# Kernel tuning notes

Hardware: AMD Instinct MI355X
Metric: run time of the kernel (lower is better)

## Reference

```python
import jax, jax.numpy as jnp
import numpy as np

T, B, D, H = 1024, 8, 1024, 16
NH = D // H  # 64, per-head width (nhid)
W_SCALE = 0.02


def setup_inputs() -> dict:
    key = jax.random.key(0)
    ks = jax.random.split(key, 10)
    return {
        "input_tensor": jax.random.normal(ks[0], (T, B, D), jnp.float32),
        "keys_vector": jax.random.normal(ks[1], (T, B, D), jnp.float32),
        "values_vector": jax.random.normal(ks[2], (T, B, D), jnp.float32),
        # per-head projection weights: [H, D, NH]
        "Wq": jax.random.normal(ks[3], (H, D, NH), jnp.float32) * W_SCALE,
        "bq": jnp.zeros((H, NH), jnp.float32),
        "Wk": jax.random.normal(ks[4], (H, D, NH), jnp.float32) * W_SCALE,
        "bk": jnp.zeros((H, NH), jnp.float32),
        "Wv": jax.random.normal(ks[5], (H, D, NH), jnp.float32) * W_SCALE,
        "bv": jnp.zeros((H, NH), jnp.float32),
        # output projection after concatenating heads
        "Wo": jax.random.normal(ks[6], (D, D), jnp.float32) * W_SCALE,
        "bo": jnp.zeros((D,), jnp.float32),
        "mask": 1,  # True: causal (growing key slice per timestep)
    }


def reference(input_tensor, keys_vector, values_vector, Wq, bq, Wk, bk, Wv, bv, Wo, bo, mask):
    # Vectorized equivalent of the per-timestep loop: query at step t attends
    # to keys/values[:t+1] when mask is set, else to the full sequence.
    q = jnp.einsum('tbd,hdk->tbhk', input_tensor, Wq) + bq   # [T,B,H,NH]
    k = jnp.einsum('sbd,hdk->sbhk', keys_vector, Wk) + bk    # [T,B,H,NH]
    v = jnp.einsum('sbd,hdk->sbhk', values_vector, Wv) + bv  # [T,B,H,NH]

    scale = 1.0 / jnp.sqrt(jnp.float32(NH))
    scores = jnp.einsum('tbhk,sbhk->bhts', q, k) * scale     # [B,H,T,T]
    if mask:
        causal = jnp.tril(jnp.ones((T, T), dtype=bool))      # s <= t
        scores = jnp.where(causal[None, None], scores, jnp.float32(-1e9))
    attn = jax.nn.softmax(scores, axis=-1)                   # over key dim s

    out = jnp.einsum('bhts,sbhk->tbhk', attn, v)             # [T,B,H,NH]
    out = out.reshape(T, B, D)                               # concat heads
    return out @ Wo.T + bo                                   # [T,B,D]
```

## Files before the change

### kernel.cpp

```cpp
#include <hip/hip_runtime.h>

typedef short bf16x8 __attribute__((ext_vector_type(8)));
typedef float f32x4 __attribute__((ext_vector_type(4)));
typedef float f32x16 __attribute__((ext_vector_type(16)));

typedef const __attribute__((address_space(1))) void* gptr_t;
typedef __attribute__((address_space(3))) void* sptr_t;

#define Z16 {0.f,0.f,0.f,0.f,0.f,0.f,0.f,0.f,0.f,0.f,0.f,0.f,0.f,0.f,0.f,0.f}
#define VMCNT(n) asm volatile("s_waitcnt vmcnt(" #n ")" ::: "memory")
#define LGKM0 asm volatile("s_waitcnt lgkmcnt(0)" ::: "memory")
#define SCHEDB __builtin_amdgcn_sched_barrier(0)
#define SBAR __builtin_amdgcn_s_barrier()

__device__ __forceinline__ void glds16(const void* g, void* s) {
  __builtin_amdgcn_global_load_lds((gptr_t)g, (sptr_t)s, 16, 0, 0);
}

__device__ __forceinline__ unsigned short f2bf(float x) {
  unsigned u = __float_as_uint(x);
  u = u + 0x7fffu + ((u >> 16) & 1u);
  return (unsigned short)(u >> 16);
}

__device__ __forceinline__ unsigned packbf(float lo, float hi) {
  return (unsigned)f2bf(lo) | (((unsigned)f2bf(hi)) << 16);
}

__global__ void cvtall(const float* __restrict__ X, const float* __restrict__ KY,
                       const float* __restrict__ VY, const float* __restrict__ Wo,
                       unsigned short* __restrict__ XB, unsigned short* __restrict__ WOB) {
  int stride = gridDim.x * blockDim.x;
  for (int i = blockIdx.x * blockDim.x + threadIdx.x; i < 6553600; i += stride) {
    const float* in; unsigned short* out; int k;
    if (i < 2097152)      { in = X;  out = XB;            k = i; }
    else if (i < 4194304) { in = KY; out = XB + 8388608;  k = i - 2097152; }
    else if (i < 6291456) { in = VY; out = XB + 16777216; k = i - 4194304; }
    else                  { in = Wo; out = WOB;           k = i - 6291456; }
    float4 v = ((const float4*)in)[k];
    uint2 r;
    r.x = packbf(v.x, v.y);
    r.y = packbf(v.z, v.w);
    ((uint2*)out)[k] = r;
  }
}

__global__ __launch_bounds__(256) void wtrans(const float* __restrict__ Wq,
                                              const float* __restrict__ Wk,
                                              const float* __restrict__ Wv,
                                              unsigned short* __restrict__ WT) {
  int m = blockIdx.y >> 4, h = blockIdx.y & 15, d0 = blockIdx.x * 64;
  const float* src = (m == 0 ? Wq : (m == 1 ? Wk : Wv)) + (size_t)h * 65536;
  __shared__ float tile[64][65];
  int c = (threadIdx.x & 15) * 4, r0 = threadIdx.x >> 4;
#pragma unroll
  for (int rr = 0; rr < 4; ++rr) {
    int dr = rr * 16 + r0;
    float4 v = *(const float4*)(src + (size_t)(d0 + dr) * 64 + c);
    tile[dr][c + 0] = v.x; tile[dr][c + 1] = v.y;
    tile[dr][c + 2] = v.z; tile[dr][c + 3] = v.w;
  }
  __syncthreads();
#pragma unroll
  for (int rr = 0; rr < 4; ++rr) {
    int kr = rr * 16 + r0;
    uint2 pk;
    pk.x = packbf(tile[c + 0][kr], tile[c + 1][kr]);
    pk.y = packbf(tile[c + 2][kr], tile[c + 3][kr]);
    *(uint2*)(WT + ((size_t)(m * 1024 + h * 64 + kr)) * 1024 + d0 + c) = pk;
  }
}

__global__ __launch_bounds__(256) void gemm_qkv(const unsigned short* __restrict__ Ab,
                                                const unsigned short* __restrict__ Bb,
                                                const float* __restrict__ bi0,
                                                const float* __restrict__ bi1,
                                                const float* __restrict__ bi2,
                                                unsigned short* __restrict__ outp) {
  const int K = 1024;
  int z = blockIdx.z;
  const unsigned short* A = Ab + (size_t)z * 8192 * 1024;
  const unsigned short* BT = Bb + (size_t)z * 1024 * 1024;
  const float* bias = z == 0 ? bi0 : (z == 1 ? bi1 : bi2);
  int lin = blockIdx.y * 64 + blockIdx.x;
  int mt = (lin & 7) * 8 + ((lin >> 3) & 7);
  int nt = lin >> 6;
  int m0 = mt * 128, n0 = nt * 128;
  __shared__ __align__(16) char lds[65536];
  int tid = threadIdx.x, w = tid >> 6, l = tid & 63, ml = l & 15, hi = l >> 4;
  int wr = (w >> 1) * 64, wc = (w & 1) * 64;
  int srow = l >> 3;
  int kphys = (l & 7) << 4;
  f32x4 acc[4][4] = {};
#pragma unroll
  for (int i = 0; i < 4; ++i) {
    int c = w * 4 + i;
    int row = c * 8 + srow;
    int klog = kphys ^ ((row & 7) << 4);
    glds16((const char*)(A + (size_t)(m0 + row) * K) + klog, lds + c * 1024);
    glds16((const char*)(BT + (size_t)(n0 + row) * K) + klog, lds + 16384 + c * 1024);
  }
  __syncthreads();
  int cur = 0;
  for (int kt16 = 0; kt16 < 16; ++kt16) {
    if (kt16 + 1 < 16) {
      char* nb = lds + (cur ^ 1) * 32768;
      int kt = (kt16 + 1) * 64;
#pragma unroll
      for (int i = 0; i < 4; ++i) {
        int c = w * 4 + i;
        int row = c * 8 + srow;
        int klog = kphys ^ ((row & 7) << 4);
        glds16((const char*)(A + (size_t)(m0 + row) * K + kt) + klog, nb + c * 1024);
        glds16((const char*)(BT + (size_t)(n0 + row) * K + kt) + klog, nb + 16384 + c * 1024);
      }
    }
    char* As = lds + cur * 32768;
    char* Bs = As + 16384;
#pragma unroll
    for (int ks = 0; ks < 2; ++ks) {
      bf16x8 af[4], bfr[4];
#pragma unroll
      for (int mi = 0; mi < 4; ++mi) {
        int row = wr + mi * 16 + ml;
        af[mi] = *(const bf16x8*)(As + row * 128 + ((ks * 64 + (hi << 4)) ^ ((row & 7) << 4)));
      }
#pragma unroll
      for (int ni = 0; ni < 4; ++ni) {
        int row = wc + ni * 16 + ml;
        bfr[ni] = *(const bf16x8*)(Bs + row * 128 + ((ks * 64 + (hi << 4)) ^ ((row & 7) << 4)));
      }
      __builtin_amdgcn_s_setprio(1);
#pragma unroll
      for (int mi = 0; mi < 4; ++mi)
#pragma unroll
        for (int ni = 0; ni < 4; ++ni)
          acc[mi][ni] = __builtin_amdgcn_mfma_f32_16x16x32_bf16(af[mi], bfr[ni], acc[mi][ni], 0, 0, 0);
      __builtin_amdgcn_s_setprio(0);
    }
    __syncthreads();
    cur ^= 1;
  }
#pragma unroll
  for (int mi = 0; mi < 4; ++mi) {
#pragma unroll
    for (int ni = 0; ni < 4; ++ni) {
      int col = wc + ni * 16 + ml;
      float bv = bias[n0 + col];
#pragma unroll
      for (int r = 0; r < 4; ++r) {
        int row = wr + mi * 16 + (hi << 2) + r;
        float v = acc[mi][ni][r] + bv;
        float pv = __shfl_xor(v, 1);
        unsigned pk = (ml & 1) ? packbf(pv, v) : packbf(v, pv);
        *(unsigned*)(lds + row * 256 + (((col * 2) & ~3) ^ ((row & 7) << 4))) = pk;
      }
    }
  }
  __syncthreads();
  unsigned short* ob = outp + (size_t)z * 8388608;
  if (z != 2) {
    int rr = tid >> 1, hh = tid & 1;
    int t = (m0 + rr) >> 3, b = (m0 + rr) & 7;
    int hg = (n0 >> 6) + hh;
    unsigned short* dst = ob + (size_t)(b * 16 + hg) * 65536 + (size_t)t * 64;
#pragma unroll
    for (int j = 0; j < 8; ++j) {
      uint4 d = *(uint4*)(lds + rr * 256 + ((hh * 128 + j * 16) ^ ((rr & 7) << 4)));
      *(uint4*)(dst + j * 8) = d;
    }
  } else {
    int t0 = m0 >> 3;
#pragma unroll
    for (int q = 0; q < 4; ++q) {
      int run = q * 256 + tid;
      int k = run & 63;
      int bh2 = run >> 6;
      int b = bh2 >> 1, hh = bh2 & 1;
      int colb = (hh * 64 + k) * 2;
      union { unsigned short u[16]; uint4 v[2]; } tmp;
#pragma unroll
      for (int tp = 0; tp < 16; ++tp) {
        int rowt = tp * 8 + b;
        tmp.u[tp] = *(unsigned short*)(lds + rowt * 256 + (colb ^ ((b & 7) << 4)));
      }
      int hg = (n0 >> 6) + hh;
      unsigned short* dst = ob + (size_t)(b * 16 + hg) * 65536 + (size_t)k * 1024 + t0;
      *(uint4*)dst = tmp.v[0];
      *(uint4*)(dst + 8) = tmp.v[1];
    }
  }
}

__global__ __launch_bounds__(256) void gemm_out(const unsigned short* __restrict__ A,
                                                const unsigned short* __restrict__ BT,
                                                const float* __restrict__ bias,
                                                float* __restrict__ outp) {
  const int K = 1024;
  int lin = blockIdx.y * 64 + blockIdx.x;
  int mt = (lin & 7) * 8 + ((lin >> 3) & 7);
  int nt = lin >> 6;
  int m0 = mt * 128, n0 = nt * 128;
  __shared__ __align__(16) char lds[65536];
  int tid = threadIdx.x, w = tid >> 6, l = tid & 63, ml = l & 15, hi = l >> 4;
  int wr = (w >> 1) * 64, wc = (w & 1) * 64;
  int srow = l >> 3;
  int kphys = (l & 7) << 4;
  f32x4 acc[4][4] = {};
#pragma unroll
  for (int i = 0; i < 4; ++i) {
    int c = w * 4 + i;
    int row = c * 8 + srow;
    int klog = kphys ^ ((row & 7) << 4);
    glds16((const char*)(A + (size_t)(m0 + row) * K) + klog, lds + c * 1024);
    glds16((const char*)(BT + (size_t)(n0 + row) * K) + klog, lds + 16384 + c * 1024);
  }
  __syncthreads();
  int cur = 0;
  for (int kt16 = 0; kt16 < 16; ++kt16) {
    if (kt16 + 1 < 16) {
      char* nb = lds + (cur ^ 1) * 32768;
      int kt = (kt16 + 1) * 64;
#pragma unroll
      for (int i = 0; i < 4; ++i) {
        int c = w * 4 + i;
        int row = c * 8 + srow;
        int klog = kphys ^ ((row & 7) << 4);
        glds16((const char*)(A + (size_t)(m0 + row) * K + kt) + klog, nb + c * 1024);
        glds16((const char*)(BT + (size_t)(n0 + row) * K + kt) + klog, nb + 16384 + c * 1024);
      }
    }
    char* As = lds + cur * 32768;
    char* Bs = As + 16384;
#pragma unroll
    for (int ks = 0; ks < 2; ++ks) {
      bf16x8 af[4], bfr[4];
#pragma unroll
      for (int mi = 0; mi < 4; ++mi) {
        int row = wr + mi * 16 + ml;
        af[mi] = *(const bf16x8*)(As + row * 128 + ((ks * 64 + (hi << 4)) ^ ((row & 7) << 4)));
      }
#pragma unroll
      for (int ni = 0; ni < 4; ++ni) {
        int row = wc + ni * 16 + ml;
        bfr[ni] = *(const bf16x8*)(Bs + row * 128 + ((ks * 64 + (hi << 4)) ^ ((row & 7) << 4)));
      }
      __builtin_amdgcn_s_setprio(1);
#pragma unroll
      for (int mi = 0; mi < 4; ++mi)
#pragma unroll
        for (int ni = 0; ni < 4; ++ni)
          acc[mi][ni] = __builtin_amdgcn_mfma_f32_16x16x32_bf16(af[mi], bfr[ni], acc[mi][ni], 0, 0, 0);
      __builtin_amdgcn_s_setprio(0);
    }
    __syncthreads();
    cur ^= 1;
  }
#pragma unroll
  for (int mi = 0; mi < 4; ++mi) {
#pragma unroll
    for (int ni = 0; ni < 4; ++ni) {
      int col = n0 + wc + ni * 16 + ml;
      float bv = bias[col];
#pragma unroll
      for (int r = 0; r < 4; ++r) {
        int row = m0 + wr + mi * 16 + (hi << 2) + r;
        outp[(size_t)row * 1024 + col] = acc[mi][ni][r] + bv;
      }
    }
  }
}

__global__ __launch_bounds__(512, 4) void attn_k(const unsigned short* __restrict__ Qp,
                                                 const unsigned short* __restrict__ Kp,
                                                 const unsigned short* __restrict__ VTp,
                                                 unsigned short* __restrict__ Op,
                                                 const int* __restrict__ maskp) {
  int lin = blockIdx.x;
  int xcd = lin & 7, idx = lin >> 3;
  int bh = xcd + 8 * (idx >> 2);
  int j = idx & 3;
  const size_t base = (size_t)bh * 65536;
  int tid = threadIdx.x, w = tid >> 6, l = tid & 63;
  int ml5 = l & 31, hi1 = l >> 5;
  int half = w & 1, pi = w >> 1;
  int stripe = (pi == 0) ? j : (pi == 1) ? (15 - j) : (pi == 2) ? (7 - j) : (8 + j);
  int tw0 = stripe * 64 + half * 32;
  int t_glob = tw0 + ml5;
  __shared__ __align__(16) char lds[32768];
  int msk = *maskp;
  const float CE = 0.18033688011112042f;
  bf16x8 bq[4];
#pragma unroll
  for (int kd = 0; kd < 4; ++kd)
    bq[kd] = *(const bf16x8*)(Qp + base + (size_t)t_glob * 64 + kd * 16 + hi1 * 8);
  f32x16 o0 = Z16, o1 = Z16;
  float m_run = -3e38f, l_run = 0.f;
  int nt = msk ? (16 - j) : 16;
  int diag = stripe;
  int srow = l >> 3, kphys = (l & 7) << 4;
  int row = w * 8 + srow;
  int klog = kphys ^ (srow << 4);
  int swz = (ml5 & 7) << 4;
  glds16((const char*)(Kp + base + (size_t)row * 64) + klog, lds + w * 1024);
  glds16((const char*)(VTp + base + (size_t)row * 1024) + klog, lds + 8192 + w * 1024);
  int cur = 0;
  for (int st = 0; st < nt; ++st) {
    if (st + 1 < nt) {
      char* nb = lds + (cur ^ 1) * 16384;
      glds16((const char*)(Kp + base + (size_t)((st + 1) * 64 + row) * 64) + klog, nb + w * 1024);
      glds16((const char*)(VTp + base + (size_t)row * 1024 + (st + 1) * 64) + klog, nb + 8192 + w * 1024);
      VMCNT(4);
    } else {
      VMCNT(0);
    }
    SCHEDB; SBAR; SCHEDB;
    if (!msk || st <= diag) {
      char* Ks = lds + cur * 16384;
      char* Vs = Ks + 8192;
      f32x16 s0 = Z16, s1 = Z16;
      __builtin_amdgcn_s_setprio(1);
#pragma unroll
      for (int kd = 0; kd < 4; ++kd) {
        int koff = kd * 32 + hi1 * 16;
        bf16x8 a0 = *(const bf16x8*)(Ks + ml5 * 128 + (koff ^ swz));
        bf16x8 a1 = *(const bf16x8*)(Ks + (32 + ml5) * 128 + (koff ^ swz));
        s0 = __builtin_amdgcn_mfma_f32_32x32x16_bf16(a0, bq[kd], s0, 0, 0, 0);
        s1 = __builtin_amdgcn_mfma_f32_32x32x16_bf16(a1, bq[kd], s1, 0, 0, 0);
      }
      __builtin_amdgcn_s_setprio(0);
      if (msk && st == diag) {
#pragma unroll
        for (int r = 0; r < 16; ++r) {
          int sl = st * 64 + (r & 3) + 8 * (r >> 2) + 4 * hi1;
          if (sl > t_glob) s0[r] = -1e30f;
          if (sl + 32 > t_glob) s1[r] = -1e30f;
        }
      }
      float t8[8];
#pragma unroll
      for (int r = 0; r < 8; ++r)
        t8[r] = fmaxf(fmaxf(s0[r], s0[r + 8]), fmaxf(s1[r], s1[r + 8]));
      float tm = fmaxf(fmaxf(fmaxf(t8[0], t8[1]), fmaxf(t8[2], t8[3])),
                       fmaxf(fmaxf(t8[4], t8[5]), fmaxf(t8[6], t8[7])));
      tm = fmaxf(tm, __shfl_xor(tm, 32));
      if (!__all(tm <= m_run + 8.0f)) {
        float m_new = fmaxf(m_run, tm);
        float sc2 = exp2f((m_run - m_new) * CE);
        l_run *= sc2;
#pragma unroll
        for (int r = 0; r < 16; ++r) { o0[r] *= sc2; o1[r] *= sc2; }
        m_run = m_new;
      }
      float mC = m_run * CE;
#pragma unroll
      for (int r = 0; r < 16; ++r) {
        s0[r] = exp2f(fmaf(s0[r], CE, -mC));
        s1[r] = exp2f(fmaf(s1[r], CE, -mC));
      }
      float a8[8];
#pragma unroll
      for (int r = 0; r < 8; ++r)
        a8[r] = (s0[r] + s0[r + 8]) + (s1[r] + s1[r + 8]);
      float ps = ((a8[0] + a8[1]) + (a8[2] + a8[3])) + ((a8[4] + a8[5]) + (a8[6] + a8[7]));
      ps += __shfl_xor(ps, 32);
      l_run += ps;
      unsigned cc0[4][2], cc1[4][2];
#pragma unroll
      for (int q = 0; q < 4; ++q) {
        cc0[q][0] = packbf(s0[4 * q + 0], s0[4 * q + 1]);
        cc0[q][1] = packbf(s0[4 * q + 2], s0[4 * q + 3]);
        cc1[q][0] = packbf(s1[4 * q + 0], s1[4 * q + 1]);
        cc1[q][1] = packbf(s1[4 * q + 2], s1[4 * q + 3]);
      }
#define CCa(a, p) ((a) < 4 ? cc0[(a) & 3][p] : cc1[(a) & 3][p])
      union U4 { unsigned u[4]; bf16x8 v; };
      bf16x8 pb[4];
#pragma unroll
      for (int kb = 0; kb < 4; ++kb) {
        U4 t;
#pragma unroll
        for (int p = 0; p < 2; ++p) {
          unsigned x = CCa(2 * kb, p), y = CCa(2 * kb + 1, p);
          unsigned v = hi1 ? x : y;
          unsigned wv = hi1 ? y : x;
          unsigned vs = __shfl_xor(v, 32);
          t.u[p]     = hi1 ? vs : wv;
          t.u[2 + p] = hi1 ? wv : vs;
        }
        pb[kb] = t.v;
      }
#undef CCa
      __builtin_amdgcn_s_setprio(1);
#pragma unroll
      for (int kb = 0; kb < 4; ++kb) {
        int koff = kb * 32 + hi1 * 16;
        bf16x8 v0 = *(const bf16x8*)(Vs + ml5 * 128 + (koff ^ swz));
        bf16x8 v1 = *(const bf16x8*)(Vs + (32 + ml5) * 128 + (koff ^ swz));
        o0 = __builtin_amdgcn_mfma_f32_32x32x16_bf16(v0, pb[kb], o0, 0, 0, 0);
        o1 = __builtin_amdgcn_mfma_f32_32x32x16_bf16(v1, pb[kb], o1, 0, 0, 0);
      }
      __builtin_amdgcn_s_setprio(0);
    }
    SCHEDB; LGKM0; SBAR;
    cur ^= 1;
  }
  float rl = 1.0f / l_run;
  int b = bh >> 4, h = bh & 15;
  unsigned short* orow = Op + (size_t)(t_glob * 8 + b) * 1024 + h * 64;
#pragma unroll
  for (int q2 = 0; q2 < 4; ++q2) {
    uint2 pk0, pk1;
    pk0.x = packbf(o0[4 * q2 + 0] * rl, o0[4 * q2 + 1] * rl);
    pk0.y = packbf(o0[4 * q2 + 2] * rl, o0[4 * q2 + 3] * rl);
    *(uint2*)(orow + 4 * hi1 + 8 * q2) = pk0;
    pk1.x = packbf(o1[4 * q2 + 0] * rl, o1[4 * q2 + 1] * rl);
    pk1.y = packbf(o1[4 * q2 + 2] * rl, o1[4 * q2 + 3] * rl);
    *(uint2*)(orow + 32 + 4 * hi1 + 8 * q2) = pk1;
  }
}

extern "C" void kernel_launch(void* const* d_in, const int* in_sizes, int n_in,
                              void* d_out, int out_size, void* d_ws, size_t ws_size,
                              hipStream_t stream) {
  const float* X  = (const float*)d_in[0];
  const float* KY = (const float*)d_in[1];
  const float* VY = (const float*)d_in[2];
  const float* Wq = (const float*)d_in[3];
  const float* bq = (const float*)d_in[4];
  const float* Wk = (const float*)d_in[5];
  const float* bk = (const float*)d_in[6];
  const float* Wv = (const float*)d_in[7];
  const float* bv = (const float*)d_in[8];
  const float* Wo = (const float*)d_in[9];
  const float* bo = (const float*)d_in[10];
  const int* mask = (const int*)d_in[11];
  char* ws = (char*)d_ws;
  unsigned short* XB  = (unsigned short*)(ws);
  unsigned short* WT  = (unsigned short*)(ws + 48ll * 1024 * 1024);
  unsigned short* WOB = (unsigned short*)(ws + 54ll * 1024 * 1024);
  unsigned short* QP  = (unsigned short*)(ws + 56ll * 1024 * 1024);
  unsigned short* OP  = (unsigned short*)(ws + 104ll * 1024 * 1024);

  cvtall<<<2048, 256, 0, stream>>>(X, KY, VY, Wo, XB, WOB);
  wtrans<<<dim3(16, 48), 256, 0, stream>>>(Wq, Wk, Wv, WT);
  gemm_qkv<<<dim3(64, 8, 3), 256, 0, stream>>>(XB, WT, bq, bk, bv, QP);
  attn_k<<<512, 512, 0, stream>>>(QP, QP + 8388608, QP + 16777216, OP, mask);
  gemm_out<<<dim3(64, 8, 1), 256, 0, stream>>>(OP, WOB, bo, (float*)d_out);
}
```

Baseline: 193.8 us.

## Drop LDS staging in attention, read K/V fragments directly from global; merge prep kernels

The attention kernel no longer stages K and V tiles into double-buffered LDS with block barriers. Each wave now loads its MFMA operands straight from global memory and depends on L1/L2 for reuse. Waves in a block now run their own number of key steps with no barrier sync, which cuts synchronisation and lets waves with short causal ranges finish early. The cost is more global and cache traffic, plus exposed load latency with no software prefetch. Separately, the bf16 conversion and weight-transpose kernels are merged into one launch to save a kernel launch.

```diff
diff --git a/kernel.cpp b/kernel.cpp
--- a/kernel.cpp
+++ b/kernel.cpp
@@ -8,10 +8,6 @@
 typedef __attribute__((address_space(3))) void* sptr_t;
 
 #define Z16 {0.f,0.f,0.f,0.f,0.f,0.f,0.f,0.f,0.f,0.f,0.f,0.f,0.f,0.f,0.f,0.f}
-#define VMCNT(n) asm volatile("s_waitcnt vmcnt(" #n ")" ::: "memory")
-#define LGKM0 asm volatile("s_waitcnt lgkmcnt(0)" ::: "memory")
-#define SCHEDB __builtin_amdgcn_sched_barrier(0)
-#define SBAR __builtin_amdgcn_s_barrier()
 
 __device__ __forceinline__ void glds16(const void* g, void* s) {
   __builtin_amdgcn_global_load_lds((gptr_t)g, (sptr_t)s, 16, 0, 0);
@@ -27,31 +23,37 @@
   return (unsigned)f2bf(lo) | (((unsigned)f2bf(hi)) << 16);
 }
 
-__global__ void cvtall(const float* __restrict__ X, const float* __restrict__ KY,
-                       const float* __restrict__ VY, const float* __restrict__ Wo,
-                       unsigned short* __restrict__ XB, unsigned short* __restrict__ WOB) {
-  int stride = gridDim.x * blockDim.x;
-  for (int i = blockIdx.x * blockDim.x + threadIdx.x; i < 6553600; i += stride) {
-    const float* in; unsigned short* out; int k;
-    if (i < 2097152)      { in = X;  out = XB;            k = i; }
-    else if (i < 4194304) { in = KY; out = XB + 8388608;  k = i - 2097152; }
-    else if (i < 6291456) { in = VY; out = XB + 16777216; k = i - 4194304; }
-    else                  { in = Wo; out = WOB;           k = i - 6291456; }
-    float4 v = ((const float4*)in)[k];
-    uint2 r;
-    r.x = packbf(v.x, v.y);
-    r.y = packbf(v.z, v.w);
-    ((uint2*)out)[k] = r;
-  }
-}
-
-__global__ __launch_bounds__(256) void wtrans(const float* __restrict__ Wq,
-                                              const float* __restrict__ Wk,
-                                              const float* __restrict__ Wv,
-                                              unsigned short* __restrict__ WT) {
-  int m = blockIdx.y >> 4, h = blockIdx.y & 15, d0 = blockIdx.x * 64;
+__global__ __launch_bounds__(256) void prep(const float* __restrict__ X,
+                                            const float* __restrict__ KY,
+                                            const float* __restrict__ VY,
+                                            const float* __restrict__ Wo,
+                                            const float* __restrict__ Wq,
+                                            const float* __restrict__ Wk,
+                                            const float* __restrict__ Wv,
+                                            unsigned short* __restrict__ XB,
+                                            unsigned short* __restrict__ WOB,
+                                            unsigned short* __restrict__ WT) {
+  __shared__ float tile[64][65];
+  if (blockIdx.x < 2048) {
+    int stride = 2048 * 256;
+    for (int i = blockIdx.x * 256 + threadIdx.x; i < 6553600; i += stride) {
+      const float* in; unsigned short* out; int k;
+      if (i < 2097152)      { in = X;  out = XB;            k = i; }
+      else if (i < 4194304) { in = KY; out = XB + 8388608;  k = i - 2097152; }
+      else if (i < 6291456) { in = VY; out = XB + 16777216; k = i - 4194304; }
+      else                  { in = Wo; out = WOB;           k = i - 6291456; }
+      float4 v = ((const float4*)in)[k];
+      uint2 r;
+      r.x = packbf(v.x, v.y);
+      r.y = packbf(v.z, v.w);
+      ((uint2*)out)[k] = r;
+    }
+    return;
+  }
+  int idx = blockIdx.x - 2048;
+  int bx = idx & 15, by = idx >> 4;
+  int m = by >> 4, h = by & 15, d0 = bx * 64;
   const float* src = (m == 0 ? Wq : (m == 1 ? Wk : Wv)) + (size_t)h * 65536;
-  __shared__ float tile[64][65];
   int c = (threadIdx.x & 15) * 4, r0 = threadIdx.x >> 4;
 #pragma unroll
   for (int rr = 0; rr < 4; ++rr) {
@@ -287,7 +289,6 @@
   int stripe = (pi == 0) ? j : (pi == 1) ? (15 - j) : (pi == 2) ? (7 - j) : (8 + j);
   int tw0 = stripe * 64 + half * 32;
   int t_glob = tw0 + ml5;
-  __shared__ __align__(16) char lds[32768];
   int msk = *maskp;
   const float CE = 0.18033688011112042f;
   bf16x8 bq[4];
@@ -296,114 +297,93 @@
     bq[kd] = *(const bf16x8*)(Qp + base + (size_t)t_glob * 64 + kd * 16 + hi1 * 8);
   f32x16 o0 = Z16, o1 = Z16;
   float m_run = -3e38f, l_run = 0.f;
-  int nt = msk ? (16 - j) : 16;
-  int diag = stripe;
-  int srow = l >> 3, kphys = (l & 7) << 4;
-  int row = w * 8 + srow;
-  int klog = kphys ^ (srow << 4);
-  int swz = (ml5 & 7) << 4;
-  glds16((const char*)(Kp + base + (size_t)row * 64) + klog, lds + w * 1024);
-  glds16((const char*)(VTp + base + (size_t)row * 1024) + klog, lds + 8192 + w * 1024);
-  int cur = 0;
-  for (int st = 0; st < nt; ++st) {
-    if (st + 1 < nt) {
-      char* nb = lds + (cur ^ 1) * 16384;
-      glds16((const char*)(Kp + base + (size_t)((st + 1) * 64 + row) * 64) + klog, nb + w * 1024);
-      glds16((const char*)(VTp + base + (size_t)row * 1024 + (st + 1) * 64) + klog, nb + 8192 + w * 1024);
-      VMCNT(4);
-    } else {
-      VMCNT(0);
-    }
-    SCHEDB; SBAR; SCHEDB;
-    if (!msk || st <= diag) {
-      char* Ks = lds + cur * 16384;
-      char* Vs = Ks + 8192;
-      f32x16 s0 = Z16, s1 = Z16;
-      __builtin_amdgcn_s_setprio(1);
-#pragma unroll
-      for (int kd = 0; kd < 4; ++kd) {
-        int koff = kd * 32 + hi1 * 16;
-        bf16x8 a0 = *(const bf16x8*)(Ks + ml5 * 128 + (koff ^ swz));
-        bf16x8 a1 = *(const bf16x8*)(Ks + (32 + ml5) * 128 + (koff ^ swz));
-        s0 = __builtin_amdgcn_mfma_f32_32x32x16_bf16(a0, bq[kd], s0, 0, 0, 0);
-        s1 = __builtin_amdgcn_mfma_f32_32x32x16_bf16(a1, bq[kd], s1, 0, 0, 0);
-      }
-      __builtin_amdgcn_s_setprio(0);
-      if (msk && st == diag) {
-#pragma unroll
-        for (int r = 0; r < 16; ++r) {
-          int sl = st * 64 + (r & 3) + 8 * (r >> 2) + 4 * hi1;
-          if (sl > t_glob) s0[r] = -1e30f;
-          if (sl + 32 > t_glob) s1[r] = -1e30f;
-        }
-      }
-      float t8[8];
-#pragma unroll
-      for (int r = 0; r < 8; ++r)
-        t8[r] = fmaxf(fmaxf(s0[r], s0[r + 8]), fmaxf(s1[r], s1[r + 8]));
-      float tm = fmaxf(fmaxf(fmaxf(t8[0], t8[1]), fmaxf(t8[2], t8[3])),
-                       fmaxf(fmaxf(t8[4], t8[5]), fmaxf(t8[6], t8[7])));
-      tm = fmaxf(tm, __shfl_xor(tm, 32));
-      if (!__all(tm <= m_run + 8.0f)) {
-        float m_new = fmaxf(m_run, tm);
-        float sc2 = exp2f((m_run - m_new) * CE);
-        l_run *= sc2;
-#pragma unroll
-        for (int r = 0; r < 16; ++r) { o0[r] *= sc2; o1[r] *= sc2; }
-        m_run = m_new;
-      }
-      float mC = m_run * CE;
+  int lim = msk ? stripe : 15;
+  const unsigned short* krow = Kp + base + (size_t)ml5 * 64 + hi1 * 8;
+  const unsigned short* vrow = VTp + base + (size_t)ml5 * 1024 + hi1 * 8;
+  for (int st = 0; st <= lim; ++st) {
+    f32x16 s0 = Z16, s1 = Z16;
+    const unsigned short* ka = krow + st * 4096;
+    __builtin_amdgcn_s_setprio(1);
+#pragma unroll
+    for (int kd = 0; kd < 4; ++kd) {
+      bf16x8 a0 = *(const bf16x8*)(ka + kd * 16);
+      bf16x8 a1 = *(const bf16x8*)(ka + 2048 + kd * 16);
+      s0 = __builtin_amdgcn_mfma_f32_32x32x16_bf16(a0, bq[kd], s0, 0, 0, 0);
+      s1 = __builtin_amdgcn_mfma_f32_32x32x16_bf16(a1, bq[kd], s1, 0, 0, 0);
+    }
+    __builtin_amdgcn_s_setprio(0);
+    if (msk && st == stripe) {
 #pragma unroll
       for (int r = 0; r < 16; ++r) {
-        s0[r] = exp2f(fmaf(s0[r], CE, -mC));
-        s1[r] = exp2f(fmaf(s1[r], CE, -mC));
-      }
-      float a8[8];
-#pragma unroll
-      for (int r = 0; r < 8; ++r)
-        a8[r] = (s0[r] + s0[r + 8]) + (s1[r] + s1[r + 8]);
-      float ps = ((a8[0] + a8[1]) + (a8[2] + a8[3])) + ((a8[4] + a8[5]) + (a8[6] + a8[7]));
-      ps += __shfl_xor(ps, 32);
-      l_run += ps;
-      unsigned cc0[4][2], cc1[4][2];
-#pragma unroll
-      for (int q = 0; q < 4; ++q) {
-        cc0[q][0] = packbf(s0[4 * q + 0], s0[4 * q + 1]);
-        cc0[q][1] = packbf(s0[4 * q + 2], s0[4 * q + 3]);
-        cc1[q][0] = packbf(s1[4 * q + 0], s1[4 * q + 1]);
-        cc1[q][1] = packbf(s1[4 * q + 2], s1[4 * q + 3]);
-      }
+        int sl = st * 64 + (r & 3) + 8 * (r >> 2) + 4 * hi1;
+        if (sl > t_glob) s0[r] = -1e30f;
+        if (sl + 32 > t_glob) s1[r] = -1e30f;
+      }
+    }
+    float t8[8];
+#pragma unroll
+    for (int r = 0; r < 8; ++r)
+      t8[r] = fmaxf(fmaxf(s0[r], s0[r + 8]), fmaxf(s1[r], s1[r + 8]));
+    float tm = fmaxf(fmaxf(fmaxf(t8[0], t8[1]), fmaxf(t8[2], t8[3])),
+                     fmaxf(fmaxf(t8[4], t8[5]), fmaxf(t8[6], t8[7])));
+    tm = fmaxf(tm, __shfl_xor(tm, 32));
+    if (!__all(tm <= m_run + 8.0f)) {
+      float m_new = fmaxf(m_run, tm);
+      float sc2 = exp2f((m_run - m_new) * CE);
+      l_run *= sc2;
+#pragma unroll
+      for (int r = 0; r < 16; ++r) { o0[r] *= sc2; o1[r] *= sc2; }
+      m_run = m_new;
+    }
+    float mC = m_run * CE;
+#pragma unroll
+    for (int r = 0; r < 16; ++r) {
+      s0[r] = exp2f(fmaf(s0[r], CE, -mC));
+      s1[r] = exp2f(fmaf(s1[r], CE, -mC));
+    }
+    float a8[8];
+#pragma unroll
+    for (int r = 0; r < 8; ++r)
+      a8[r] = (s0[r] + s0[r + 8]) + (s1[r] + s1[r + 8]);
+    float ps = ((a8[0] + a8[1]) + (a8[2] + a8[3])) + ((a8[4] + a8[5]) + (a8[6] + a8[7]));
+    ps += __shfl_xor(ps, 32);
+    l_run += ps;
+    unsigned cc0[4][2], cc1[4][2];
+#pragma unroll
+    for (int q = 0; q < 4; ++q) {
+      cc0[q][0] = packbf(s0[4 * q + 0], s0[4 * q + 1]);
+      cc0[q][1] = packbf(s0[4 * q + 2], s0[4 * q + 3]);
+      cc1[q][0] = packbf(s1[4 * q + 0], s1[4 * q + 1]);
+      cc1[q][1] = packbf(s1[4 * q + 2], s1[4 * q + 3]);
+    }
 #define CCa(a, p) ((a) < 4 ? cc0[(a) & 3][p] : cc1[(a) & 3][p])
-      union U4 { unsigned u[4]; bf16x8 v; };
-      bf16x8 pb[4];
-#pragma unroll
-      for (int kb = 0; kb < 4; ++kb) {
-        U4 t;
-#pragma unroll
-        for (int p = 0; p < 2; ++p) {
-          unsigned x = CCa(2 * kb, p), y = CCa(2 * kb + 1, p);
-          unsigned v = hi1 ? x : y;
-          unsigned wv = hi1 ? y : x;
-          unsigned vs = __shfl_xor(v, 32);
-          t.u[p]     = hi1 ? vs : wv;
-          t.u[2 + p] = hi1 ? wv : vs;
-        }
-        pb[kb] = t.v;
-      }
+    union U4 { unsigned u[4]; bf16x8 v; };
+    bf16x8 pb[4];
+#pragma unroll
+    for (int kb = 0; kb < 4; ++kb) {
+      U4 t;
+#pragma unroll
+      for (int p = 0; p < 2; ++p) {
+        unsigned x = CCa(2 * kb, p), y = CCa(2 * kb + 1, p);
+        unsigned v = hi1 ? x : y;
+        unsigned wv = hi1 ? y : x;
+        unsigned vs = __shfl_xor(v, 32);
+        t.u[p]     = hi1 ? vs : wv;
+        t.u[2 + p] = hi1 ? wv : vs;
+      }
+      pb[kb] = t.v;
+    }
 #undef CCa
-      __builtin_amdgcn_s_setprio(1);
-#pragma unroll
-      for (int kb = 0; kb < 4; ++kb) {
-        int koff = kb * 32 + hi1 * 16;
-        bf16x8 v0 = *(const bf16x8*)(Vs + ml5 * 128 + (koff ^ swz));
-        bf16x8 v1 = *(const bf16x8*)(Vs + (32 + ml5) * 128 + (koff ^ swz));
-        o0 = __builtin_amdgcn_mfma_f32_32x32x16_bf16(v0, pb[kb], o0, 0, 0, 0);
-        o1 = __builtin_amdgcn_mfma_f32_32x32x16_bf16(v1, pb[kb], o1, 0, 0, 0);
-      }
-      __builtin_amdgcn_s_setprio(0);
-    }
-    SCHEDB; LGKM0; SBAR;
-    cur ^= 1;
+    const unsigned short* va = vrow + st * 64;
+    __builtin_amdgcn_s_setprio(1);
+#pragma unroll
+    for (int kb = 0; kb < 4; ++kb) {
+      bf16x8 v0 = *(const bf16x8*)(va + kb * 16);
+      bf16x8 v1 = *(const bf16x8*)(va + 32768 + kb * 16);
+      o0 = __builtin_amdgcn_mfma_f32_32x32x16_bf16(v0, pb[kb], o0, 0, 0, 0);
+      o1 = __builtin_amdgcn_mfma_f32_32x32x16_bf16(v1, pb[kb], o1, 0, 0, 0);
+    }
+    __builtin_amdgcn_s_setprio(0);
   }
   float rl = 1.0f / l_run;
   int b = bh >> 4, h = bh & 15;
@@ -442,8 +422,7 @@
   unsigned short* QP  = (unsigned short*)(ws + 56ll * 1024 * 1024);
   unsigned short* OP  = (unsigned short*)(ws + 104ll * 1024 * 1024);
 
-  cvtall<<<2048, 256, 0, stream>>>(X, KY, VY, Wo, XB, WOB);
-  wtrans<<<dim3(16, 48), 256, 0, stream>>>(Wq, Wk, Wv, WT);
+  prep<<<2816, 256, 0, stream>>>(X, KY, VY, Wo, Wq, Wk, Wv, XB, WOB, WT);
   gemm_qkv<<<dim3(64, 8, 3), 256, 0, stream>>>(XB, WT, bq, bk, bv, QP);
   attn_k<<<512, 512, 0, stream>>>(QP, QP + 8388608, QP + 16777216, OP, mask);
   gemm_out<<<dim3(64, 8, 1), 256, 0, stream>>>(OP, WOB, bo, (float*)d_out);
```

After: 211.3 us. +9.0%, slower.
